# Optimization experiments

Hardware: AMD Instinct MI355X
Metric: run time of the kernel (lower is better)

The kernel has to match this reference:

```python
import jax, jax.numpy as jnp
import numpy as np

N_PTS = 800000
PLANE = 512
FDIM = 16


def setup_inputs() -> dict:
    key = jax.random.key(0)
    k1, k2 = jax.random.split(key)
    x = jax.random.uniform(k1, (N_PTS, 3), dtype=jnp.float32)
    # learned tri-plane features, init U(-0.01, 0.01) as in init_parameters
    fm = jax.random.uniform(k2, (3, PLANE, PLANE, FDIM), dtype=jnp.float32,
                            minval=-0.01, maxval=0.01)
    return {"x": x, "fm": fm}


def reference(x, fm):
    # x: [N,3] in [0,1]; fm: [3,H,W,C] tri-plane textures
    N = x.shape[0]
    _, H, W, C = fm.shape
    # decompose xyz into the three plane uv coords: (yz), (xz), (xy)
    dx = jnp.stack([x[:, (1, 2)], x[:, (0, 2)], x[:, (0, 1)]], axis=0)  # [3,N,2]
    # nvdiffrast texture convention: u along W, v along H, texel centers at (i+0.5)/W
    u = dx[..., 0] * W - 0.5  # [3,N]
    v = dx[..., 1] * H - 0.5
    i0f = jnp.floor(u)
    j0f = jnp.floor(v)
    fu = u - i0f  # bilinear fractions, [3,N]
    fv = v - j0f
    i0 = jnp.clip(i0f.astype(jnp.int32), 0, W - 1)  # clamp boundary mode
    i1 = jnp.clip(i0f.astype(jnp.int32) + 1, 0, W - 1)
    j0 = jnp.clip(j0f.astype(jnp.int32), 0, H - 1)
    j1 = jnp.clip(j0f.astype(jnp.int32) + 1, 0, H - 1)
    p = jnp.arange(3)[:, None]  # plane index, broadcasts against [3,N]
    t00 = fm[p, j0, i0]  # [3,N,C]
    t01 = fm[p, j0, i1]
    t10 = fm[p, j1, i0]
    t11 = fm[p, j1, i1]
    w00 = ((1.0 - fv) * (1.0 - fu))[..., None]
    w01 = ((1.0 - fv) * fu)[..., None]
    w10 = (fv * (1.0 - fu))[..., None]
    w11 = (fv * fu)[..., None]
    enc = w00 * t00 + w01 * t01 + w10 * t10 + w11 * t11  # [3,N,C]
    # permute(1,2,0,3).view(N, 3*C) on [3,N,1,C] == transpose to [N,3,C] then flatten
    return enc.transpose(1, 0, 2).reshape(N, 3 * C)
```

## Files before the change

kernel.cpp:

```cpp
#include <hip/hip_runtime.h>
#include <hip/hip_bf16.h>


#define N_PTS 800000
#define PLANE 512
#define FDIM  16
#define FM_ELEMS (3 * PLANE * PLANE * FDIM)
#define FMH_BYTES (FM_ELEMS * 2)
#define GATHER_THREADS (N_PTS * 8)
#define TOTAL_F32 (N_PTS * 48)

typedef _Float16 half2v __attribute__((ext_vector_type(2)));
typedef _Float16 half4v __attribute__((ext_vector_type(4)));
typedef float    float2v __attribute__((ext_vector_type(2)));

__global__ __launch_bounds__(256) void convert_fp16_kernel(
    const float* __restrict__ fm, _Float16* __restrict__ fmh)
{
    unsigned t = blockIdx.x * blockDim.x + threadIdx.x;
    float4 v = ((const float4*)fm)[t];
    half4v h;
    h.x = (_Float16)v.x; h.y = (_Float16)v.y;
    h.z = (_Float16)v.z; h.w = (_Float16)v.w;
    ((half4v*)fmh)[t] = h;
}

__global__ __launch_bounds__(256) void trimip_fp16_fused_kernel(
    const float* __restrict__ x,
    const _Float16* __restrict__ fmh,
    float* __restrict__ out)
{
    unsigned t = blockIdx.x * blockDim.x + threadIdx.x;
    if (t >= (unsigned)GATHER_THREADS) return;

    unsigned c2 = t & 7u;
    unsigned n  = t >> 3;

    const float* xr = x + 3u * n;
    float x0 = __builtin_nontemporal_load(xr + 0);
    float x1 = __builtin_nontemporal_load(xr + 1);
    float x2 = __builtin_nontemporal_load(xr + 2);

    float ua[3] = {x1, x0, x0};
    float va[3] = {x2, x2, x1};

    float fu[3], fv[3];
    unsigned o00[3], o01[3], o10[3], o11[3];

#pragma unroll
    for (int p = 0; p < 3; ++p) {
        float u = ua[p] * (float)PLANE - 0.5f;
        float v = va[p] * (float)PLANE - 0.5f;
        float i0f = floorf(u);
        float j0f = floorf(v);
        fu[p] = u - i0f;
        fv[p] = v - j0f;

        int i0 = (int)i0f;
        int j0 = (int)j0f;
        int i1 = min(max(i0 + 1, 0), PLANE - 1);
        int j1 = min(max(j0 + 1, 0), PLANE - 1);
        i0 = min(max(i0, 0), PLANE - 1);
        j0 = min(max(j0, 0), PLANE - 1);

        unsigned pb = (unsigned)p * (PLANE * PLANE * FDIM) + 2u * c2;
        o00[p] = pb + (unsigned)(j0 * PLANE + i0) * FDIM;
        o01[p] = pb + (unsigned)(j0 * PLANE + i1) * FDIM;
        o10[p] = pb + (unsigned)(j1 * PLANE + i0) * FDIM;
        o11[p] = pb + (unsigned)(j1 * PLANE + i1) * FDIM;
    }

    half2v h00[3], h01[3], h10[3], h11[3];
#pragma unroll
    for (int p = 0; p < 3; ++p) {
        h00[p] = *(const half2v*)(fmh + o00[p]);
        h01[p] = *(const half2v*)(fmh + o01[p]);
        h10[p] = *(const half2v*)(fmh + o10[p]);
        h11[p] = *(const half2v*)(fmh + o11[p]);
    }

    float2v* ob = (float2v*)out + (size_t)n * 24u + c2;
#pragma unroll
    for (int p = 0; p < 3; ++p) {
        float2v r;
        {
            float t00 = (float)h00[p].x, t01 = (float)h01[p].x;
            float t10 = (float)h10[p].x, t11 = (float)h11[p].x;
            float r0 = t00 + fu[p] * (t01 - t00);
            float r1 = t10 + fu[p] * (t11 - t10);
            r.x = r0 + fv[p] * (r1 - r0);
        }
        {
            float t00 = (float)h00[p].y, t01 = (float)h01[p].y;
            float t10 = (float)h10[p].y, t11 = (float)h11[p].y;
            float r0 = t00 + fu[p] * (t01 - t00);
            float r1 = t10 + fu[p] * (t11 - t10);
            r.y = r0 + fv[p] * (r1 - r0);
        }
        __builtin_nontemporal_store(r, ob + (unsigned)p * 8u);
    }
}

__global__ __launch_bounds__(256) void trimip_f32_kernel(
    const float* __restrict__ x,
    const float* __restrict__ fm,
    float* __restrict__ out)
{
    unsigned t = blockIdx.x * blockDim.x + threadIdx.x;
    if (t >= (unsigned)TOTAL_F32) return;

    unsigned c    = t & 15u;
    unsigned unit = t >> 4;
    unsigned n    = unit / 3u;
    unsigned p    = unit - n * 3u;

    unsigned iu = (p == 0u) ? 1u : 0u;
    unsigned iv = (p == 2u) ? 1u : 2u;

    float a = x[n * 3u + iu];
    float b = x[n * 3u + iv];

    float u = a * (float)PLANE - 0.5f;
    float v = b * (float)PLANE - 0.5f;
    float i0f = floorf(u);
    float j0f = floorf(v);
    float fu = u - i0f;
    float fv = v - j0f;

    int i0 = (int)i0f;
    int j0 = (int)j0f;
    int i1 = min(max(i0 + 1, 0), PLANE - 1);
    int j1 = min(max(j0 + 1, 0), PLANE - 1);
    i0 = min(max(i0, 0), PLANE - 1);
    j0 = min(max(j0, 0), PLANE - 1);

    const float* base = fm + (size_t)p * (PLANE * PLANE * FDIM);
    float t00 = base[((size_t)(j0 * PLANE + i0)) * FDIM + c];
    float t01 = base[((size_t)(j0 * PLANE + i1)) * FDIM + c];
    float t10 = base[((size_t)(j1 * PLANE + i0)) * FDIM + c];
    float t11 = base[((size_t)(j1 * PLANE + i1)) * FDIM + c];

    float r0 = t00 + fu * (t01 - t00);
    float r1 = t10 + fu * (t11 - t10);
    float r  = r0 + fv * (r1 - r0);

    __builtin_nontemporal_store(r, &out[t]);
}

extern "C" void kernel_launch(void* const* d_in, const int* in_sizes, int n_in,
                              void* d_out, int out_size, void* d_ws, size_t ws_size,
                              hipStream_t stream)
{
    const float* x  = (const float*)d_in[0];
    const float* fm = (const float*)d_in[1];
    float* out      = (float*)d_out;

    if (ws_size >= (size_t)FMH_BYTES) {
        _Float16* fmh = (_Float16*)d_ws;
        convert_fp16_kernel<<<FM_ELEMS / 4 / 256, 256, 0, stream>>>(fm, fmh);
        trimip_fp16_fused_kernel<<<(GATHER_THREADS + 255) / 256, 256, 0, stream>>>(x, fmh, out);
    } else {
        trimip_f32_kernel<<<(TOTAL_F32 + 255) / 256, 256, 0, stream>>>(x, fm, out);
    }
}
```

Baseline: 285.5 us.

## Bin points by coarse Morton key before gathering to improve texture cache locality

Adds a counting-sort pipeline (zero histogram, atomic histogram over 4096 Morton bins, single-block prefix scan, atomic scatter) that reorders points spatially into a workspace buffer. The gather kernel then reads the sorted records, writes results to each point's original index, and uses a block-index swizzle. The goal is to turn the random texel gathers into clustered accesses with better L2/cache reuse. In exchange it adds four extra launches, global atomics, and scattered output writes. It only runs when the workspace is large enough, and otherwise falls back to the old path.

```diff
diff --git a/kernel.cpp b/kernel.cpp
--- a/kernel.cpp
+++ b/kernel.cpp
@@ -7,7 +7,16 @@
 #define FDIM  16
 #define FM_ELEMS (3 * PLANE * PLANE * FDIM)
 #define FMH_BYTES (FM_ELEMS * 2)
+#define NBINS 4096
+#define HIST_BYTES (NBINS * 4)
+#define SORTED_BYTES (N_PTS * 16)
+#define WS_FMH_OFF 0
+#define WS_HIST_OFF FMH_BYTES
+#define WS_SORT_OFF (FMH_BYTES + HIST_BYTES)
+#define WS_TOTAL (WS_SORT_OFF + SORTED_BYTES)
 #define GATHER_THREADS (N_PTS * 8)
+#define GATHER_BLOCKS (GATHER_THREADS / 256)
+#define PT_BLOCKS (N_PTS / 256)
 #define TOTAL_F32 (N_PTS * 48)
 
 typedef _Float16 half2v __attribute__((ext_vector_type(2)));
@@ -18,6 +27,7 @@
     const float* __restrict__ fm, _Float16* __restrict__ fmh)
 {
     unsigned t = blockIdx.x * blockDim.x + threadIdx.x;
+    if (t >= (unsigned)(FM_ELEMS / 4)) return;
     float4 v = ((const float4*)fm)[t];
     half4v h;
     h.x = (_Float16)v.x; h.y = (_Float16)v.y;
@@ -25,21 +35,95 @@
     ((half4v*)fmh)[t] = h;
 }
 
-__global__ __launch_bounds__(256) void trimip_fp16_fused_kernel(
-    const float* __restrict__ x,
+__global__ __launch_bounds__(256) void zero_hist_kernel(unsigned* __restrict__ hist)
+{
+    unsigned t = blockIdx.x * blockDim.x + threadIdx.x;
+    if (t < NBINS) hist[t] = 0u;
+}
+
+__device__ __forceinline__ unsigned spread4(unsigned v)
+{
+    return (v & 1u) | ((v & 2u) << 2) | ((v & 4u) << 4) | ((v & 8u) << 6);
+}
+
+__device__ __forceinline__ unsigned morton_key(float x0, float x1, float x2)
+{
+    int ix = min(max((int)(x0 * 16.0f), 0), 15);
+    int iy = min(max((int)(x1 * 16.0f), 0), 15);
+    int iz = min(max((int)(x2 * 16.0f), 0), 15);
+    return spread4((unsigned)ix) | (spread4((unsigned)iy) << 1)
+         | (spread4((unsigned)iz) << 2);
+}
+
+__global__ __launch_bounds__(256) void hist_kernel(
+    const float* __restrict__ x, unsigned* __restrict__ hist)
+{
+    unsigned t = blockIdx.x * blockDim.x + threadIdx.x;
+    if (t >= (unsigned)N_PTS) return;
+    float x0 = x[3u * t + 0u];
+    float x1 = x[3u * t + 1u];
+    float x2 = x[3u * t + 2u];
+    atomicAdd(&hist[morton_key(x0, x1, x2)], 1u);
+}
+
+__global__ __launch_bounds__(1024) void prefix_kernel(unsigned* __restrict__ hist)
+{
+    __shared__ unsigned s[1024];
+    unsigned t = threadIdx.x;
+    unsigned v0 = hist[4u * t + 0u];
+    unsigned v1 = hist[4u * t + 1u];
+    unsigned v2 = hist[4u * t + 2u];
+    unsigned v3 = hist[4u * t + 3u];
+    unsigned sum = v0 + v1 + v2 + v3;
+    s[t] = sum;
+    __syncthreads();
+    for (unsigned off = 1u; off < 1024u; off <<= 1) {
+        unsigned add = (t >= off) ? s[t - off] : 0u;
+        __syncthreads();
+        s[t] += add;
+        __syncthreads();
+    }
+    unsigned base = s[t] - sum;
+    hist[4u * t + 0u] = base;
+    hist[4u * t + 1u] = base + v0;
+    hist[4u * t + 2u] = base + v0 + v1;
+    hist[4u * t + 3u] = base + v0 + v1 + v2;
+}
+
+__global__ __launch_bounds__(256) void scatter_kernel(
+    const float* __restrict__ x, unsigned* __restrict__ hist,
+    float4* __restrict__ sorted)
+{
+    unsigned t = blockIdx.x * blockDim.x + threadIdx.x;
+    if (t >= (unsigned)N_PTS) return;
+    float x0 = x[3u * t + 0u];
+    float x1 = x[3u * t + 1u];
+    float x2 = x[3u * t + 2u];
+    unsigned pos = atomicAdd(&hist[morton_key(x0, x1, x2)], 1u);
+    if (pos < (unsigned)N_PTS) {
+        float4 rec;
+        rec.x = x0; rec.y = x1; rec.z = x2; rec.w = __uint_as_float(t);
+        sorted[pos] = rec;
+    }
+}
+
+__global__ __launch_bounds__(256) void trimip_fp16_sorted_kernel(
+    const float4* __restrict__ sorted,
     const _Float16* __restrict__ fmh,
     float* __restrict__ out)
 {
-    unsigned t = blockIdx.x * blockDim.x + threadIdx.x;
+    unsigned bid = blockIdx.x;
+    unsigned swz = (bid & 7u) * (GATHER_BLOCKS / 8u) + (bid >> 3);
+    unsigned t = swz * 256u + threadIdx.x;
     if (t >= (unsigned)GATHER_THREADS) return;
 
     unsigned c2 = t & 7u;
-    unsigned n  = t >> 3;
-
-    const float* xr = x + 3u * n;
-    float x0 = __builtin_nontemporal_load(xr + 0);
-    float x1 = __builtin_nontemporal_load(xr + 1);
-    float x2 = __builtin_nontemporal_load(xr + 2);
+    unsigned s  = t >> 3;
+
+    float4 rec = sorted[s];
+    float x0 = rec.x, x1 = rec.y, x2 = rec.z;
+    unsigned n = __float_as_uint(rec.w);
+    if (n >= (unsigned)N_PTS) return;
 
     float ua[3] = {x1, x0, x0};
     float va[3] = {x2, x2, x1};
@@ -101,6 +185,80 @@
     }
 }
 
+__global__ __launch_bounds__(256) void trimip_fp16_fused_kernel(
+    const float* __restrict__ x,
+    const _Float16* __restrict__ fmh,
+    float* __restrict__ out)
+{
+    unsigned t = blockIdx.x * blockDim.x + threadIdx.x;
+    if (t >= (unsigned)GATHER_THREADS) return;
+
+    unsigned c2 = t & 7u;
+    unsigned n  = t >> 3;
+
+    const float* xr = x + 3u * n;
+    float x0 = xr[0], x1 = xr[1], x2 = xr[2];
+
+    float ua[3] = {x1, x0, x0};
+    float va[3] = {x2, x2, x1};
+
+    float fu[3], fv[3];
+    unsigned o00[3], o01[3], o10[3], o11[3];
+
+#pragma unroll
+    for (int p = 0; p < 3; ++p) {
+        float u = ua[p] * (float)PLANE - 0.5f;
+        float v = va[p] * (float)PLANE - 0.5f;
+        float i0f = floorf(u);
+        float j0f = floorf(v);
+        fu[p] = u - i0f;
+        fv[p] = v - j0f;
+
+        int i0 = (int)i0f;
+        int j0 = (int)j0f;
+        int i1 = min(max(i0 + 1, 0), PLANE - 1);
+        int j1 = min(max(j0 + 1, 0), PLANE - 1);
+        i0 = min(max(i0, 0), PLANE - 1);
+        j0 = min(max(j0, 0), PLANE - 1);
+
+        unsigned pb = (unsigned)p * (PLANE * PLANE * FDIM) + 2u * c2;
+        o00[p] = pb + (unsigned)(j0 * PLANE + i0) * FDIM;
+        o01[p] = pb + (unsigned)(j0 * PLANE + i1) * FDIM;
+        o10[p] = pb + (unsigned)(j1 * PLANE + i0) * FDIM;
+        o11[p] = pb + (unsigned)(j1 * PLANE + i1) * FDIM;
+    }
+
+    half2v h00[3], h01[3], h10[3], h11[3];
+#pragma unroll
+    for (int p = 0; p < 3; ++p) {
+        h00[p] = *(const half2v*)(fmh + o00[p]);
+        h01[p] = *(const half2v*)(fmh + o01[p]);
+        h10[p] = *(const half2v*)(fmh + o10[p]);
+        h11[p] = *(const half2v*)(fmh + o11[p]);
+    }
+
+    float2v* ob = (float2v*)out + (size_t)n * 24u + c2;
+#pragma unroll
+    for (int p = 0; p < 3; ++p) {
+        float2v r;
+        {
+            float t00 = (float)h00[p].x, t01 = (float)h01[p].x;
+            float t10 = (float)h10[p].x, t11 = (float)h11[p].x;
+            float r0 = t00 + fu[p] * (t01 - t00);
+            float r1 = t10 + fu[p] * (t11 - t10);
+            r.x = r0 + fv[p] * (r1 - r0);
+        }
+        {
+            float t00 = (float)h00[p].y, t01 = (float)h01[p].y;
+            float t10 = (float)h10[p].y, t11 = (float)h11[p].y;
+            float r0 = t00 + fu[p] * (t01 - t00);
+            float r1 = t10 + fu[p] * (t11 - t10);
+            r.y = r0 + fv[p] * (r1 - r0);
+        }
+        __builtin_nontemporal_store(r, ob + (unsigned)p * 8u);
+    }
+}
+
 __global__ __launch_bounds__(256) void trimip_f32_kernel(
     const float* __restrict__ x,
     const float* __restrict__ fm,
@@ -155,7 +313,19 @@
     const float* fm = (const float*)d_in[1];
     float* out      = (float*)d_out;
 
-    if (ws_size >= (size_t)FMH_BYTES) {
+    if (ws_size >= (size_t)WS_TOTAL) {
+        char* ws = (char*)d_ws;
+        _Float16* fmh  = (_Float16*)(ws + WS_FMH_OFF);
+        unsigned* hist = (unsigned*)(ws + WS_HIST_OFF);
+        float4*  sorted = (float4*)(ws + WS_SORT_OFF);
+
+        convert_fp16_kernel<<<FM_ELEMS / 4 / 256, 256, 0, stream>>>(fm, fmh);
+        zero_hist_kernel<<<NBINS / 256, 256, 0, stream>>>(hist);
+        hist_kernel<<<PT_BLOCKS, 256, 0, stream>>>(x, hist);
+        prefix_kernel<<<1, 1024, 0, stream>>>(hist);
+        scatter_kernel<<<PT_BLOCKS, 256, 0, stream>>>(x, hist, sorted);
+        trimip_fp16_sorted_kernel<<<GATHER_BLOCKS, 256, 0, stream>>>(sorted, fmh, out);
+    } else if (ws_size >= (size_t)FMH_BYTES) {
         _Float16* fmh = (_Float16*)d_ws;
         convert_fp16_kernel<<<FM_ELEMS / 4 / 256, 256, 0, stream>>>(fm, fmh);
         trimip_fp16_fused_kernel<<<(GATHER_THREADS + 255) / 256, 256, 0, stream>>>(x, fmh, out);
```

Result: slower. 336.5 us (+17.9%).
